# Optimization experiments

Measured on AMD Instinct MI355X. Metric: run time of the kernel, lower is better.

Reference implementation:

```python
import jax, jax.numpy as jnp
import numpy as np
from functools import partial

BANK = 256
ADDR = 64
OUT_C, IN_C, KH, KW = 64, 64, 3, 3
BS, H, W = 32, 128, 128


def setup_inputs() -> dict:
    key = jax.random.key(0)
    ks = jax.random.split(key, 6)
    x = jax.random.normal(ks[0], (BS, IN_C, H, W), dtype=jnp.float32)
    w_addr = jax.random.normal(ks[1], (BS, ADDR), dtype=jnp.float32)
    b_addr = jax.random.normal(ks[2], (BS, OUT_C, ADDR), dtype=jnp.float32)
    # learned parameters
    w_bank = jax.random.normal(ks[3], (BANK, OUT_C, IN_C, KH, KW), dtype=jnp.float32) * (1.0 / np.sqrt(IN_C * KH * KW))
    bound = 1.0 / np.sqrt(IN_C * KH * KW)
    b_bank = jax.random.uniform(ks[4], (BANK,), minval=-bound, maxval=bound, dtype=jnp.float32)
    address_space = jax.random.normal(ks[5], (BANK, ADDR), dtype=jnp.float32)
    return {"x": x, "w_addr": w_addr, "b_addr": b_addr, "w_bank": w_bank,
            "b_bank": b_bank, "address_space": address_space, "s": 1, "p": 1}


def _hyper_conv(x, w_addr, b_addr, w_bank, b_bank, address_space, s, p):
    # soft addressing: keys @ address_space.T -> softmax -> weighted sum of bank
    sel_w = jax.nn.softmax(w_addr @ address_space.T, axis=-1)          # [bs, bank]
    w = jnp.einsum('bn,noikl->boikl', sel_w, w_bank)                   # [bs, O, I, kh, kw]
    sel_b = jax.nn.softmax(b_addr @ address_space.T, axis=-1)          # [bs, O, bank]
    b = jnp.einsum('bon,n->bo', sel_b, b_bank)                         # [bs, O]

    def conv_one(xi, wi):
        # xi: [I, H, W], wi: [O, I, kh, kw]
        return jax.lax.conv_general_dilated(
            xi[None], wi, window_strides=(s, s), padding=[(p, p), (p, p)],
            dimension_numbers=('NCHW', 'OIHW', 'NCHW'))[0]

    o = jax.vmap(conv_one)(x, w)                                       # [bs, O, H', W']
    return o + b[:, :, None, None]


def reference(x, w_addr, b_addr, w_bank, b_bank, address_space, s, p):
    return _hyper_conv(x, w_addr, b_addr, w_bank, b_bank, address_space, int(s), int(p))
```

## Files before the change

kernel.cpp:

```cpp
#include <hip/hip_runtime.h>
#include <hip/hip_bf16.h>
#include <math.h>

#define BS   32
#define IC   64
#define OC   64
#define HH   128
#define WW   128
#define BANK 256
#define ADDR 64
#define WELEM (OC*IC*9)
#define PLANE (HH*WW)

typedef short short8 __attribute__((ext_vector_type(8)));
typedef int   i32x4  __attribute__((ext_vector_type(4)));
typedef float f32x16 __attribute__((ext_vector_type(16)));

__device__ __forceinline__ short f2bf(float f) {
    unsigned u = __builtin_bit_cast(unsigned, f);
    unsigned r = (u + 0x7FFFu + ((u >> 16) & 1u)) >> 16;
    return (short)r;
}

__device__ __forceinline__ int pack_bf2(float lo, float hi) {
    unsigned ul = __builtin_bit_cast(unsigned, lo);
    unsigned uh = __builtin_bit_cast(unsigned, hi);
    unsigned rl = (ul + 0x7FFFu + ((ul >> 16) & 1u)) >> 16;
    unsigned rh = (uh + 0x7FFFu + ((uh >> 16) & 1u)) & 0xFFFF0000u;
    return (int)(rh | (rl & 0xFFFFu));
}

__global__ __launch_bounds__(BANK) void k_selw(const float* __restrict__ w_addr,
                                               const float* __restrict__ aspace,
                                               float* __restrict__ sel_w) {
    int b = blockIdx.x;
    int n = threadIdx.x;
    const float* wa = w_addr + b * ADDR;
    const float* as = aspace + n * ADDR;
    float dot = 0.f;
#pragma unroll
    for (int k = 0; k < ADDR; ++k) dot = fmaf(wa[k], as[k], dot);

    __shared__ float red[BANK];
    red[n] = dot; __syncthreads();
    for (int s = BANK / 2; s > 0; s >>= 1) {
        if (n < s) red[n] = fmaxf(red[n], red[n + s]);
        __syncthreads();
    }
    float m = red[0]; __syncthreads();
    float e = expf(dot - m);
    red[n] = e; __syncthreads();
    for (int s = BANK / 2; s > 0; s >>= 1) {
        if (n < s) red[n] += red[n + s];
        __syncthreads();
    }
    sel_w[b * BANK + n] = e / red[0];
}

__global__ __launch_bounds__(BANK) void k_bias(const float* __restrict__ b_addr,
                                               const float* __restrict__ aspace,
                                               const float* __restrict__ b_bank,
                                               float* __restrict__ bias) {
    int bo = blockIdx.x;
    int n  = threadIdx.x;
    const float* ba = b_addr + (size_t)bo * ADDR;
    const float* as = aspace + n * ADDR;
    float dot = 0.f;
#pragma unroll
    for (int k = 0; k < ADDR; ++k) dot = fmaf(ba[k], as[k], dot);

    __shared__ float red[BANK];
    red[n] = dot; __syncthreads();
    for (int s = BANK / 2; s > 0; s >>= 1) {
        if (n < s) red[n] = fmaxf(red[n], red[n + s]);
        __syncthreads();
    }
    float m = red[0]; __syncthreads();
    float e = expf(dot - m);
    red[n] = e; __syncthreads();
    for (int s = BANK / 2; s > 0; s >>= 1) {
        if (n < s) red[n] += red[n + s];
        __syncthreads();
    }
    float denom = red[0]; __syncthreads();
    red[n] = e * b_bank[n]; __syncthreads();
    for (int s = BANK / 2; s > 0; s >>= 1) {
        if (n < s) red[n] += red[n + s];
        __syncthreads();
    }
    if (n == 0) bias[bo] = red[0] / denom;
}

__global__ __launch_bounds__(256) void k_wmix(const float* __restrict__ sel_w,
                                              const float* __restrict__ w_bank,
                                              __hip_bfloat16* __restrict__ wmb) {
    __shared__ float s_red[4 * 32 * 64];

    int tid = threadIdx.x;
    int jl  = tid & 63;
    int c   = tid >> 6;
    int jb  = blockIdx.x * 64 + jl;

    int n0 = __builtin_amdgcn_readfirstlane(c * 64);
    const float* selp = sel_w + n0;

    float wv[64];
#pragma unroll
    for (int n = 0; n < 64; ++n)
        wv[n] = w_bank[(size_t)(n0 + n) * WELEM + jb];

    float acc[BS];
#pragma unroll
    for (int b = 0; b < BS; ++b) acc[b] = 0.f;
#pragma unroll
    for (int b = 0; b < BS; ++b)
#pragma unroll
        for (int n = 0; n < 64; ++n)
            acc[b] = fmaf(selp[b * BANK + n], wv[n], acc[b]);

#pragma unroll
    for (int b = 0; b < BS; ++b)
        s_red[(c * 32 + b) * 64 + jl] = acc[b];
    __syncthreads();

    int B0  = (tid * 8) & 31;
    int jl2 = (tid * 8) >> 5;
    int j   = blockIdx.x * 64 + jl2;
    int o   = j / 576;
    int rem = j - o * 576;
    int i   = rem / 9;
    int tap = rem - i * 9;
    size_t base = ((size_t)tap * 8 + (i >> 3)) * 512 + (size_t)o * 8 + (i & 7);
#pragma unroll
    for (int u = 0; u < 8; ++u) {
        int b = B0 + u;
        float v = s_red[(0 * 32 + b) * 64 + jl2] + s_red[(1 * 32 + b) * 64 + jl2]
                + s_red[(2 * 32 + b) * 64 + jl2] + s_red[(3 * 32 + b) * 64 + jl2];
        short sv = f2bf(v);
        wmb[(size_t)b * (9 * 8 * 64 * 8) + base] = *reinterpret_cast<__hip_bfloat16*>(&sv);
    }
}

__global__ __launch_bounds__(512, 4) void k_conv(const float* __restrict__ x,
                                                 const short* __restrict__ wmb,
                                                 const float* __restrict__ bias,
                                                 float* __restrict__ out) {
    __shared__ int  s_x[2][4 * 2 * 4 * 136];
    __shared__ float s_bias[OC];

    int orig    = blockIdx.x;
    int logical = (orig & 7) * 256 + (orig >> 3);
    int b    = logical >> 6;
    int y0   = (logical & 63) * 2;
    int tid  = threadIdx.x;
    int lane = tid & 63;
    int wv   = tid >> 6;
    int h    = lane >> 5;
    int ln   = lane & 31;
    int wr   = wv & 1;
    int oh   = (wv >> 1) & 1;
    int ph   = wv >> 2;

    if (tid < OC) s_bias[tid] = bias[b * OC + tid];
    if (tid < 128) {
        int buf  = tid >> 6;
        int row  = (tid & 63) >> 1;
        int slot = (tid & 1) ? 132 : 3;
        s_x[buf][row * 136 + slot] = 0;
    }

    const float* xb   = x + (size_t)b * IC * PLANE;
    const short* wmbs = wmb + (size_t)b * 36864;

    int x_goff[2], x_lds[2], x_icb[2]; bool x_ok[2];
#pragma unroll
    for (int k = 0; k < 2; ++k) {
        int u  = k * 512 + tid;
        int ky = u >> 8;
        int g  = (u >> 7) & 1;
        int p  = (u >> 5) & 3;
        int q  = u & 31;
        int gy = y0 - 1 + ky;
        x_ok[k]   = ((unsigned)gy < (unsigned)HH);
        x_icb[k]  = g * 8 + 2 * p;
        x_goff[k] = gy * WW + 4 * q;
        x_lds[k]  = ((ky * 2 + g) * 4 + p) * 136 + 4 + 4 * q;
    }

    float4 xlo[2], xhi[2];

    auto LOADX = [&](int cc) {
#pragma unroll
        for (int k = 0; k < 2; ++k) {
            if (x_ok[k]) {
                const float* p = xb + (size_t)(cc * 16 + x_icb[k]) * PLANE + x_goff[k];
                xlo[k] = *(const float4*)p;
                xhi[k] = *(const float4*)(p + PLANE);
            } else {
                xlo[k] = make_float4(0.f, 0.f, 0.f, 0.f);
                xhi[k] = make_float4(0.f, 0.f, 0.f, 0.f);
            }
        }
    };
    auto STOREX = [&](int bf) {
#pragma unroll
        for (int k = 0; k < 2; ++k) {
            i32x4 d;
#pragma unroll
            for (int j = 0; j < 4; ++j)
                d[j] = pack_bf2(((const float*)&xlo[k])[j], ((const float*)&xhi[k])[j]);
            *(i32x4*)&s_x[bf][x_lds[k]] = d;
        }
    };

    f32x16 acc[2];
    acc[0] = (f32x16)0.0f;
    acc[1] = (f32x16)0.0f;

    LOADX(0);
    STOREX(0);
    __syncthreads();

    for (int cc = 0; cc < 4; ++cc) {
        int bf = cc & 1;

        short8 areg[9];
#pragma unroll
        for (int tap = 0; tap < 9; ++tap)
            areg[tap] = *(const short8*)(wmbs +
                (size_t)((tap * 8 + 2 * cc + h) * 64 + oh * 32 + ln) * 8);

        if (cc < 3) LOADX(cc + 1);

        const int* xi = (const int*)s_x[bf];
#pragma unroll
        for (int ky = 0; ky < 3; ++ky) {
#pragma unroll
            for (int kx = 0; kx < 3; ++kx) {
                short8 a = areg[ky * 3 + kx];
#pragma unroll
                for (int nt = 0; nt < 2; ++nt) {
                    int px   = ph * 64 + nt * 32 + ln;
                    int base = (((wr + ky) * 2 + h) * 4) * 136 + px + kx + 3;
                    i32x4 d;
                    d[0] = xi[base];
                    d[1] = xi[base + 136];
                    d[2] = xi[base + 272];
                    d[3] = xi[base + 408];
                    short8 bb = __builtin_bit_cast(short8, d);
                    acc[nt] = __builtin_amdgcn_mfma_f32_32x32x16_bf16(a, bb, acc[nt], 0, 0, 0);
                }
            }
        }
        if (cc < 3) STOREX(bf ^ 1);
        __syncthreads();
    }

    int y = y0 + wr;
    float* ob = out + (size_t)b * OC * PLANE;
#pragma unroll
    for (int nt = 0; nt < 2; ++nt) {
#pragma unroll
        for (int r = 0; r < 16; ++r) {
            int oc = oh * 32 + (r & 3) + 8 * (r >> 2) + 4 * h;
            int px = ph * 64 + nt * 32 + ln;
            ob[((size_t)oc * HH + y) * WW + px] = acc[nt][r] + s_bias[oc];
        }
    }
}

extern "C" void kernel_launch(void* const* d_in, const int* in_sizes, int n_in,
                              void* d_out, int out_size, void* d_ws, size_t ws_size,
                              hipStream_t stream) {
    const float* x      = (const float*)d_in[0];
    const float* w_addr = (const float*)d_in[1];
    const float* b_addr = (const float*)d_in[2];
    const float* w_bank = (const float*)d_in[3];
    const float* b_bank = (const float*)d_in[4];
    const float* aspace = (const float*)d_in[5];
    float* out = (float*)d_out;

    char* ws = (char*)d_ws;
    float*          sel_w = (float*)ws;
    float*          bias  = (float*)(ws + 32768);
    __hip_bfloat16* wmb   = (__hip_bfloat16*)(ws + 40960);

    k_selw<<<BS, BANK, 0, stream>>>(w_addr, aspace, sel_w);
    k_bias<<<BS * OC, BANK, 0, stream>>>(b_addr, aspace, b_bank, bias);
    k_wmix<<<WELEM / 64, 256, 0, stream>>>(sel_w, w_bank, wmb);
    k_conv<<<BS * 64, 512, 0, stream>>>(x, (const short*)wmb, bias, out);
}
```

Measured before the change: 135.5 us.

## Double input-channel chunk in conv, use hardware bf16 pack, restructure bias kernel

The conv kernel now stages 32 input channels per chunk instead of 16. That halves the outer loop to two iterations and the number of block barriers, at the cost of twice the LDS for the x tile and more live A-fragment registers. The manual round-to-nearest bf16 packing is replaced by the v_cvt_pk_bf16_f32 instruction. The bias softmax kernel is rewritten so each block handles 8 output channels, with 32 threads per channel doing 8 dot products each. This cuts the launch from 2048 blocks with deep tree reductions to 256 blocks. The larger LDS footprint could lower occupancy of the conv kernel.

```diff
diff --git a/kernel.cpp b/kernel.cpp
--- a/kernel.cpp
+++ b/kernel.cpp
@@ -22,12 +22,10 @@
     return (short)r;
 }
 
-__device__ __forceinline__ int pack_bf2(float lo, float hi) {
-    unsigned ul = __builtin_bit_cast(unsigned, lo);
-    unsigned uh = __builtin_bit_cast(unsigned, hi);
-    unsigned rl = (ul + 0x7FFFu + ((ul >> 16) & 1u)) >> 16;
-    unsigned rh = (uh + 0x7FFFu + ((uh >> 16) & 1u)) & 0xFFFF0000u;
-    return (int)(rh | (rl & 0xFFFFu));
+__device__ __forceinline__ int cvt_pk_bf2(float lo, float hi) {
+    int r;
+    asm("v_cvt_pk_bf16_f32 %0, %1, %2" : "=v"(r) : "v"(lo), "v"(hi));
+    return r;
 }
 
 __global__ __launch_bounds__(BANK) void k_selw(const float* __restrict__ w_addr,
@@ -57,38 +55,57 @@
     sel_w[b * BANK + n] = e / red[0];
 }
 
-__global__ __launch_bounds__(BANK) void k_bias(const float* __restrict__ b_addr,
-                                               const float* __restrict__ aspace,
-                                               const float* __restrict__ b_bank,
-                                               float* __restrict__ bias) {
-    int bo = blockIdx.x;
-    int n  = threadIdx.x;
-    const float* ba = b_addr + (size_t)bo * ADDR;
-    const float* as = aspace + n * ADDR;
-    float dot = 0.f;
-#pragma unroll
-    for (int k = 0; k < ADDR; ++k) dot = fmaf(ba[k], as[k], dot);
-
-    __shared__ float red[BANK];
-    red[n] = dot; __syncthreads();
-    for (int s = BANK / 2; s > 0; s >>= 1) {
-        if (n < s) red[n] = fmaxf(red[n], red[n + s]);
-        __syncthreads();
-    }
-    float m = red[0]; __syncthreads();
-    float e = expf(dot - m);
-    red[n] = e; __syncthreads();
-    for (int s = BANK / 2; s > 0; s >>= 1) {
-        if (n < s) red[n] += red[n + s];
-        __syncthreads();
-    }
-    float denom = red[0]; __syncthreads();
-    red[n] = e * b_bank[n]; __syncthreads();
-    for (int s = BANK / 2; s > 0; s >>= 1) {
-        if (n < s) red[n] += red[n + s];
-        __syncthreads();
-    }
-    if (n == 0) bias[bo] = red[0] / denom;
+__global__ __launch_bounds__(256) void k_bias(const float* __restrict__ b_addr,
+                                              const float* __restrict__ aspace,
+                                              const float* __restrict__ b_bank,
+                                              float* __restrict__ bias) {
+    __shared__ float s_m[256], s_s[256], s_w[256];
+    int blk = blockIdx.x;
+    int b   = blk >> 3;
+    int og  = blk & 7;
+    int tid = threadIdx.x;
+    int ol  = tid >> 5;
+    int o   = og * 8 + ol;
+    int q   = tid & 31;
+
+    const float* ba = b_addr + ((size_t)b * OC + o) * ADDR;
+    float bav[64];
+#pragma unroll
+    for (int i = 0; i < 16; ++i)
+        *(float4*)&bav[i * 4] = *(const float4*)&ba[i * 4];
+
+    float d[8];
+#pragma unroll
+    for (int n = 0; n < 8; ++n) {
+        const float* ar = aspace + (size_t)(q * 8 + n) * ADDR;
+        float s = 0.f;
+#pragma unroll
+        for (int k = 0; k < 64; ++k) s = fmaf(bav[k], ar[k], s);
+        d[n] = s;
+    }
+    float mx = d[0];
+#pragma unroll
+    for (int n = 1; n < 8; ++n) mx = fmaxf(mx, d[n]);
+    s_m[ol * 32 + q] = mx;
+    __syncthreads();
+    float M = -1e30f;
+    for (int j = 0; j < 32; ++j) M = fmaxf(M, s_m[ol * 32 + j]);
+
+    float s = 0.f, ws = 0.f;
+#pragma unroll
+    for (int n = 0; n < 8; ++n) {
+        float e = expf(d[n] - M);
+        s += e;
+        ws += e * b_bank[q * 8 + n];
+    }
+    s_s[ol * 32 + q] = s;
+    s_w[ol * 32 + q] = ws;
+    __syncthreads();
+    if (q == 0) {
+        float S = 0.f, W = 0.f;
+        for (int j = 0; j < 32; ++j) { S += s_s[ol * 32 + j]; W += s_w[ol * 32 + j]; }
+        bias[b * OC + o] = W / S;
+    }
 }
 
 __global__ __launch_bounds__(256) void k_wmix(const float* __restrict__ sel_w,
@@ -145,7 +162,7 @@
                                                  const short* __restrict__ wmb,
                                                  const float* __restrict__ bias,
                                                  float* __restrict__ out) {
-    __shared__ int  s_x[2][4 * 2 * 4 * 136];
+    __shared__ int   s_x[2][4 * 16 * 136];
     __shared__ float s_bias[OC];
 
     int orig    = blockIdx.x;
@@ -162,9 +179,9 @@
     int ph   = wv >> 2;
 
     if (tid < OC) s_bias[tid] = bias[b * OC + tid];
-    if (tid < 128) {
-        int buf  = tid >> 6;
-        int row  = (tid & 63) >> 1;
+    if (tid < 256) {
+        int buf  = tid >> 7;
+        int row  = (tid >> 1) & 63;
         int slot = (tid & 1) ? 132 : 3;
         s_x[buf][row * 136 + slot] = 0;
     }
@@ -172,28 +189,27 @@
     const float* xb   = x + (size_t)b * IC * PLANE;
     const short* wmbs = wmb + (size_t)b * 36864;
 
-    int x_goff[2], x_lds[2], x_icb[2]; bool x_ok[2];
-#pragma unroll
-    for (int k = 0; k < 2; ++k) {
+    int x_goff[4], x_lds[4], x_P[4]; bool x_ok[4];
+#pragma unroll
+    for (int k = 0; k < 4; ++k) {
         int u  = k * 512 + tid;
-        int ky = u >> 8;
-        int g  = (u >> 7) & 1;
-        int p  = (u >> 5) & 3;
+        int ky = u >> 9;
+        int P  = (u >> 5) & 15;
         int q  = u & 31;
         int gy = y0 - 1 + ky;
         x_ok[k]   = ((unsigned)gy < (unsigned)HH);
-        x_icb[k]  = g * 8 + 2 * p;
+        x_P[k]    = P;
         x_goff[k] = gy * WW + 4 * q;
-        x_lds[k]  = ((ky * 2 + g) * 4 + p) * 136 + 4 + 4 * q;
-    }
-
-    float4 xlo[2], xhi[2];
+        x_lds[k]  = (ky * 16 + P) * 136 + 4 + 4 * q;
+    }
+
+    float4 xlo[4], xhi[4];
 
     auto LOADX = [&](int cc) {
 #pragma unroll
-        for (int k = 0; k < 2; ++k) {
+        for (int k = 0; k < 4; ++k) {
             if (x_ok[k]) {
-                const float* p = xb + (size_t)(cc * 16 + x_icb[k]) * PLANE + x_goff[k];
+                const float* p = xb + (size_t)(cc * 32 + 2 * x_P[k]) * PLANE + x_goff[k];
                 xlo[k] = *(const float4*)p;
                 xhi[k] = *(const float4*)(p + PLANE);
             } else {
@@ -204,11 +220,11 @@
     };
     auto STOREX = [&](int bf) {
 #pragma unroll
-        for (int k = 0; k < 2; ++k) {
+        for (int k = 0; k < 4; ++k) {
             i32x4 d;
 #pragma unroll
             for (int j = 0; j < 4; ++j)
-                d[j] = pack_bf2(((const float*)&xlo[k])[j], ((const float*)&xhi[k])[j]);
+                d[j] = cvt_pk_bf2(((const float*)&xlo[k])[j], ((const float*)&xhi[k])[j]);
             *(i32x4*)&s_x[bf][x_lds[k]] = d;
         }
     };
@@ -221,27 +237,29 @@
     STOREX(0);
     __syncthreads();
 
-    for (int cc = 0; cc < 4; ++cc) {
-        int bf = cc & 1;
-
-        short8 areg[9];
+#pragma unroll
+    for (int cc = 0; cc < 2; ++cc) {
+        short8 aA[9], aB[9];
 #pragma unroll
         for (int tap = 0; tap < 9; ++tap)
-            areg[tap] = *(const short8*)(wmbs +
-                (size_t)((tap * 8 + 2 * cc + h) * 64 + oh * 32 + ln) * 8);
-
-        if (cc < 3) LOADX(cc + 1);
-
-        const int* xi = (const int*)s_x[bf];
+            aA[tap] = *(const short8*)(wmbs +
+                (size_t)((tap * 8 + cc * 4 + h) * 64 + oh * 32 + ln) * 8);
+#pragma unroll
+        for (int tap = 0; tap < 9; ++tap)
+            aB[tap] = *(const short8*)(wmbs +
+                (size_t)((tap * 8 + cc * 4 + 2 + h) * 64 + oh * 32 + ln) * 8);
+
+        const int* xi = (const int*)s_x[cc];
+
 #pragma unroll
         for (int ky = 0; ky < 3; ++ky) {
 #pragma unroll
             for (int kx = 0; kx < 3; ++kx) {
-                short8 a = areg[ky * 3 + kx];
+                short8 a = aA[ky * 3 + kx];
 #pragma unroll
                 for (int nt = 0; nt < 2; ++nt) {
                     int px   = ph * 64 + nt * 32 + ln;
-                    int base = (((wr + ky) * 2 + h) * 4) * 136 + px + kx + 3;
+                    int base = ((wr + ky) * 16 + h * 4) * 136 + px + kx + 3;
                     i32x4 d;
                     d[0] = xi[base];
                     d[1] = xi[base + 136];
@@ -252,8 +270,30 @@
                 }
             }
         }
-        if (cc < 3) STOREX(bf ^ 1);
-        __syncthreads();
+        if (cc == 0) LOADX(1);
+#pragma unroll
+        for (int ky = 0; ky < 3; ++ky) {
+#pragma unroll
+            for (int kx = 0; kx < 3; ++kx) {
+                short8 a = aB[ky * 3 + kx];
+#pragma unroll
+                for (int nt = 0; nt < 2; ++nt) {
+                    int px   = ph * 64 + nt * 32 + ln;
+                    int base = ((wr + ky) * 16 + 8 + h * 4) * 136 + px + kx + 3;
+                    i32x4 d;
+                    d[0] = xi[base];
+                    d[1] = xi[base + 136];
+                    d[2] = xi[base + 272];
+                    d[3] = xi[base + 408];
+                    short8 bb = __builtin_bit_cast(short8, d);
+                    acc[nt] = __builtin_amdgcn_mfma_f32_32x32x16_bf16(a, bb, acc[nt], 0, 0, 0);
+                }
+            }
+        }
+        if (cc == 0) {
+            STOREX(1);
+            __syncthreads();
+        }
     }
 
     int y = y0 + wr;
@@ -286,7 +326,7 @@
     __hip_bfloat16* wmb   = (__hip_bfloat16*)(ws + 40960);
 
     k_selw<<<BS, BANK, 0, stream>>>(w_addr, aspace, sel_w);
-    k_bias<<<BS * OC, BANK, 0, stream>>>(b_addr, aspace, b_bank, bias);
+    k_bias<<<BS * 8, 256, 0, stream>>>(b_addr, aspace, b_bank, bias);
     k_wmix<<<WELEM / 64, 256, 0, stream>>>(sel_w, w_bank, wmb);
     k_conv<<<BS * 64, 512, 0, stream>>>(x, (const short*)wmb, bias, out);
 }
```

Result: slower. 142.4 us (+5.1%).
